# Kernel tuning notes

Hardware: AMD Instinct MI355X
Metric: run time of the kernel (lower is better)

Reference implementation:

```python
import jax, jax.numpy as jnp
import numpy as np

F_NODES = 360        # nodes per graph == num_features (square connectome)
NUM_GRAPHS = 128
NUM_EDGES = 1_000_000
C = 128              # hidden_channels
NUM_LAYERS = 3
HIDDEN = 512
NUM_CLASSES = 2
EPS = 1e-5


def _bn(x, g, b):
    # BatchNorm1d in training mode: biased batch statistics over the batch dim.
    m = x.mean(axis=0)
    v = x.var(axis=0)
    return (x - m) * jax.lax.rsqrt(v + EPS) * g + b


def _gcn(x, W, b, src, dst):
    # GCNConv: x' = D^{-1/2} (A + I) D^{-1/2} (x W) + b
    N = x.shape[0]
    h = x @ W                                   # [N, C]
    loop = jnp.arange(N, dtype=src.dtype)
    src2 = jnp.concatenate([src, loop])
    dst2 = jnp.concatenate([dst, loop])
    deg = jax.ops.segment_sum(jnp.ones_like(dst2, dtype=h.dtype), dst2, num_segments=N)
    dinv = jnp.where(deg > 0, jax.lax.rsqrt(deg), 0.0)
    norm = dinv[src2] * dinv[dst2]              # [E+N]
    out = jax.ops.segment_sum(h[src2] * norm[:, None], dst2, num_segments=N)
    return out + b


def setup_inputs() -> dict:
    key = jax.random.key(0)
    ks = jax.random.split(key, 16)
    N = NUM_GRAPHS * F_NODES
    x = jax.random.normal(ks[0], (N, F_NODES), jnp.float32)
    # edges confined within each graph
    g = jax.random.randint(ks[1], (NUM_EDGES,), 0, NUM_GRAPHS)
    edge_src = g * F_NODES + jax.random.randint(ks[2], (NUM_EDGES,), 0, F_NODES)
    edge_dst = g * F_NODES + jax.random.randint(ks[3], (NUM_EDGES,), 0, F_NODES)
    batch = jnp.repeat(jnp.arange(NUM_GRAPHS), F_NODES)

    def lin(k, fi, fo):
        s = 1.0 / np.sqrt(fi)
        return jax.random.uniform(k, (fi, fo), jnp.float32, -s, s)

    input_dim = F_NODES * (F_NODES + 1) // 2    # 64980
    input_dim1 = input_dim + C * NUM_LAYERS     # 65364
    H2 = HIDDEN // 2
    params = dict(
        Wc1=lin(ks[4], F_NODES, C), bc1=jnp.zeros((C,), jnp.float32),
        Wc2=lin(ks[5], C, C), bc2=jnp.zeros((C,), jnp.float32),
        Wc3=lin(ks[6], C, C), bc3=jnp.zeros((C,), jnp.float32),
        bn_g=jnp.ones((input_dim,), jnp.float32), bn_b=jnp.zeros((input_dim,), jnp.float32),
        bnh_g=jnp.ones((C * NUM_LAYERS,), jnp.float32), bnh_b=jnp.zeros((C * NUM_LAYERS,), jnp.float32),
        W1=lin(ks[7], input_dim1, HIDDEN), b1=jnp.zeros((HIDDEN,), jnp.float32),
        g1=jnp.ones((HIDDEN,), jnp.float32), be1=jnp.zeros((HIDDEN,), jnp.float32),
        W2=lin(ks[8], HIDDEN, H2), b2=jnp.zeros((H2,), jnp.float32),
        g2=jnp.ones((H2,), jnp.float32), be2=jnp.zeros((H2,), jnp.float32),
        W3=lin(ks[9], H2, H2), b3=jnp.zeros((H2,), jnp.float32),
        g3=jnp.ones((H2,), jnp.float32), be3=jnp.zeros((H2,), jnp.float32),
        W4=lin(ks[10], H2, NUM_CLASSES), b4=jnp.zeros((NUM_CLASSES,), jnp.float32),
    )
    return {"x": x, "edge_src": edge_src, "edge_dst": edge_dst, "batch": batch, **params}


def reference(x, edge_src, edge_dst, batch,
              Wc1, bc1, Wc2, bc2, Wc3, bc3,
              bn_g, bn_b, bnh_g, bnh_b,
              W1, b1, g1, be1, W2, b2, g2, be2, W3, b3, g3, be3, W4, b4):
    N, F = x.shape
    B = N // F                                   # nodes per graph == F
    # stacked GCN convs with tanh
    xs = [x]
    for W, b in ((Wc1, bc1), (Wc2, bc2), (Wc3, bc3)):
        xs.append(jnp.tanh(_gcn(xs[-1], W, b, edge_src, edge_dst)))
    # per-graph upper-triangular gather of the raw connectome (vectorized)
    iu0, iu1 = np.triu_indices(F)
    x0 = xs[0].reshape(B, F, F)[:, iu0, iu1]     # [B, F(F+1)/2]
    x0 = _bn(x0, bn_g, bn_b)
    # per-layer segment-mean pooling over graphs
    cnt = jax.ops.segment_sum(jnp.ones((N,), x.dtype), batch, num_segments=B)
    h = jnp.concatenate(
        [jax.ops.segment_sum(xx, batch, num_segments=B) / cnt[:, None] for xx in xs[1:]],
        axis=1)                                  # [B, C*num_layers]
    h = _bn(h, bnh_g, bnh_b)
    z = jnp.concatenate([x0, h], axis=1)         # [B, input_dim1]
    # MLP head (dropout in eval mode => identity)
    z = jax.nn.relu(_bn(z @ W1 + b1, g1, be1))
    z = jax.nn.relu(_bn(z @ W2 + b2, g2, be2))
    z = jax.nn.relu(_bn(z @ W3 + b3, g3, be3))
    return jax.nn.log_softmax(z @ W4 + b4, axis=1)
```

## Files before the change

kernel.cpp:

```cpp
#include <hip/hip_runtime.h>
#include <hip/hip_bf16.h>
#include <math.h>

#define FN 360
#define NG 128
#define NN 46080
#define CH 128
#define NE 1000000
#define TRI 64980
#define D1 65364
#define ZLD 65376
#define H1 512
#define H2 256
#define EPS 1e-5f
#define NSPLIT 64
#define NB1 720
#define ERNG 8192
#define NR 123
#define NCH 8
#define CROWS 45
#define SBCAP 32

typedef unsigned short u16;
typedef __attribute__((ext_vector_type(8))) short bf16x8;
typedef __attribute__((ext_vector_type(4))) float f32x4;

__device__ __forceinline__ float bf2f(u16 v) {
  union { unsigned u; float f; } x; x.u = ((unsigned)v) << 16; return x.f;
}
__device__ __forceinline__ u16 f2bf(float f) {
  union { float f; unsigned u; } x; x.f = f;
  unsigned r = x.u + 0x7fffu + ((x.u >> 16) & 1u);
  return (u16)(r >> 16);
}
__device__ __forceinline__ bf16x8 bzero8() {
  bf16x8 z;
#pragma unroll
  for (int j = 0; j < 8; j++) z[j] = 0;
  return z;
}

static const size_t Z_OFF    = 0;
static const size_t PART_OFF = 16736256;
static const size_t EBUF_OFF = PART_OFF;
static const size_t CNT_OFF  = PART_OFF + 16121856;
static const size_t Y1_OFF   = 50290688;
static const size_t A1_OFF   = 50552832;
static const size_t A2_OFF   = 50683904;
static const size_t A3_OFF   = 50749440;
static const size_t DEG_OFF  = 66355200;
static const size_t HP_OFF   = 66539520;
static const size_t AB_OFF   = 66740224;
static const size_t PT_OFF   = 99917824;
static const size_t H_OFF    = 111714304;

__global__ __launch_bounds__(256) void k_gemm1deg(
    const float* __restrict__ X, const float* __restrict__ W,
    u16* __restrict__ PT,
    const int* __restrict__ src, const int* __restrict__ dst,
    float* __restrict__ deg, unsigned* __restrict__ ebuf, int* __restrict__ cnt) {
  if (blockIdx.x >= NB1) {
    __shared__ int cur[NG * NCH];
    int r = blockIdx.x - NB1;
    for (int i = threadIdx.x; i < NG * NCH; i += 256) cur[i] = 0;
    __syncthreads();
    int base = r * ERNG;
#pragma unroll 4
    for (int it = 0; it < ERNG / 256; it++) {
      int e = base + it * 256 + threadIdx.x;
      if (e < NE) {
        int s = src[e], d = dst[e];
        atomicAdd(&deg[d], 1.0f);
        int g = d / FN;
        int ls = s - g * FN, ld = d - g * FN;
        int gc = g * NCH + ld / CROWS;
        int slot = atomicAdd(&cur[gc], 1);
        if (slot < SBCAP)
          ebuf[((size_t)r * (NG * NCH) + gc) * SBCAP + slot] =
              (unsigned)ls | ((unsigned)ld << 16);
      }
    }
    __syncthreads();
    for (int i = threadIdx.x; i < NG * NCH; i += 256)
      cnt[r * (NG * NCH) + i] = cur[i];
    return;
  }
  __shared__ __attribute__((aligned(16))) u16 WT[128][40];
  const int K = FN;
  int wid = threadIdx.x >> 6, lane = threadIdx.x & 63;
  int quad = lane >> 4, l16 = lane & 15;
  int m0 = blockIdx.x * 64 + (wid & 1) * 32;
  int n0w = (wid >> 1) * 64;
  int kl = threadIdx.x >> 3, nseg = (threadIdx.x & 7) * 16;
  f32x4 acc[2][4];
#pragma unroll
  for (int i = 0; i < 2; i++)
#pragma unroll
    for (int j = 0; j < 4; j++) acc[i][j] = (f32x4){0,0,0,0};
  for (int k0 = 0; k0 < K; k0 += 32) {
    __syncthreads();
    int kg = k0 + kl;
    if (kg < K) {
      const float* wrow = W + (size_t)kg * CH + nseg;
      f32x4 w0 = *(const f32x4*)(wrow);
      f32x4 w1 = *(const f32x4*)(wrow + 4);
      f32x4 w2 = *(const f32x4*)(wrow + 8);
      f32x4 w3 = *(const f32x4*)(wrow + 12);
#pragma unroll
      for (int j = 0; j < 4; j++) {
        WT[nseg + j][kl]      = f2bf(w0[j]);
        WT[nseg + 4 + j][kl]  = f2bf(w1[j]);
        WT[nseg + 8 + j][kl]  = f2bf(w2[j]);
        WT[nseg + 12 + j][kl] = f2bf(w3[j]);
      }
    } else {
#pragma unroll
      for (int j = 0; j < 16; j++) WT[nseg + j][kl] = 0;
    }
    __syncthreads();
    int kk = k0 + quad * 8;
    bool kin = kk < K;
    bf16x8 af[2];
#pragma unroll
    for (int tm = 0; tm < 2; tm++) {
      int row = m0 + tm * 16 + l16;
      bf16x8 a = bzero8();
      if (kin) {
        f32x4 va = *(const f32x4*)(X + (size_t)row * K + kk);
        f32x4 vb = *(const f32x4*)(X + (size_t)row * K + kk + 4);
#pragma unroll
        for (int j = 0; j < 4; j++) { a[j] = (short)f2bf(va[j]); a[4 + j] = (short)f2bf(vb[j]); }
      }
      af[tm] = a;
    }
    bf16x8 bfr[4];
#pragma unroll
    for (int tn = 0; tn < 4; tn++)
      bfr[tn] = *(const bf16x8*)&WT[n0w + tn * 16 + l16][quad * 8];
#pragma unroll
    for (int tm = 0; tm < 2; tm++)
#pragma unroll
      for (int tn = 0; tn < 4; tn++)
        acc[tm][tn] = __builtin_amdgcn_mfma_f32_16x16x32_bf16(af[tm], bfr[tn], acc[tm][tn], 0, 0, 0);
  }
#pragma unroll
  for (int tm = 0; tm < 2; tm++)
#pragma unroll
    for (int tn = 0; tn < 4; tn++) {
      int col = n0w + tn * 16 + l16;
      int rowb = m0 + tm * 16 + quad * 4;
#pragma unroll
      for (int r = 0; r < 4; r++) {
        int row = rowb + r;
        int g = row / FN, lr = row - g * FN;
        PT[((size_t)g * CH + col) * FN + lr] = f2bf(acc[tm][tn][r]);
      }
    }
}

__global__ __launch_bounds__(256) void k_abuild3(
    const unsigned* __restrict__ ebuf, const int* __restrict__ cnt,
    const float* __restrict__ deg, u16* __restrict__ Ab) {
  __shared__ __attribute__((aligned(16))) float sA[CROWS * FN];
  __shared__ int scnt[NR];
  int g = blockIdx.x >> 3, ch = blockIdx.x & 7;
  int gc = g * NCH + ch;
  int r0 = ch * CROWS;
  for (int i = threadIdx.x; i < CROWS * FN / 4; i += 256) ((f32x4*)sA)[i] = (f32x4){0,0,0,0};
  for (int i = threadIdx.x; i < NR; i += 256) scnt[i] = cnt[i * (NG * NCH) + gc];
  __syncthreads();
  const float* dg = deg + g * FN;
  for (int idx = threadIdx.x; idx < NR * SBCAP; idx += 256) {
    int r = idx >> 5, sl = idx & (SBCAP - 1);
    if (sl < scnt[r]) {
      unsigned p = ebuf[((size_t)r * (NG * NCH) + gc) * SBCAP + sl];
      int ls = (int)(p & 0xffffu), ld = (int)(p >> 16);
      float w = rsqrtf(dg[ls] + 1.0f) * rsqrtf(dg[ld] + 1.0f);
      atomicAdd(&sA[(ld - r0) * FN + ls], w);
    }
  }
  __syncthreads();
  if (threadIdx.x < CROWS) {
    int l = r0 + threadIdx.x;
    float dv = rsqrtf(dg[l] + 1.0f);
    sA[threadIdx.x * FN + l] += dv * dv;
  }
  __syncthreads();
  unsigned* dstu = (unsigned*)(Ab + (size_t)g * FN * FN + (size_t)r0 * FN);
  for (int i = threadIdx.x; i < CROWS * FN / 2; i += 256) {
    unsigned lo = f2bf(sA[2 * i]), hi = f2bf(sA[2 * i + 1]);
    dstu[i] = lo | (hi << 16);
  }
}

template<bool GUARD>
__device__ __forceinline__ void gbig_body(
    const u16* __restrict__ Z, const float* __restrict__ W1f,
    float* __restrict__ part, int s, int n0b) {
  __shared__ __attribute__((aligned(16))) u16 WT[128][40];
  int wid = threadIdx.x >> 6, lane = threadIdx.x & 63;
  int quad = lane >> 4, l16 = lane & 15;
  int m0 = wid * 32;
  int kl = threadIdx.x >> 3, nseg = (threadIdx.x & 7) * 16;
  int kbeg = s * 1024;
  int kend = GUARD ? ((ZLD < kbeg + 1024) ? ZLD : (kbeg + 1024)) : (kbeg + 1024);
  f32x4 acc[2][8];
#pragma unroll
  for (int i = 0; i < 2; i++)
#pragma unroll
    for (int j = 0; j < 8; j++) acc[i][j] = (f32x4){0,0,0,0};
  for (int k0 = kbeg; k0 < kend; k0 += 32) {
    __syncthreads();
    int kg = k0 + kl;
    if (!GUARD || kg < D1) {
      const float* wrow = W1f + (size_t)kg * H1 + n0b + nseg;
      f32x4 w0 = *(const f32x4*)(wrow);
      f32x4 w1 = *(const f32x4*)(wrow + 4);
      f32x4 w2 = *(const f32x4*)(wrow + 8);
      f32x4 w3 = *(const f32x4*)(wrow + 12);
#pragma unroll
      for (int j = 0; j < 4; j++) {
        WT[nseg + j][kl]      = f2bf(w0[j]);
        WT[nseg + 4 + j][kl]  = f2bf(w1[j]);
        WT[nseg + 8 + j][kl]  = f2bf(w2[j]);
        WT[nseg + 12 + j][kl] = f2bf(w3[j]);
      }
    } else {
#pragma unroll
      for (int j = 0; j < 16; j++) WT[nseg + j][kl] = 0;
    }
    __syncthreads();
    int kk = k0 + quad * 8;
    bf16x8 af[2];
#pragma unroll
    for (int tm = 0; tm < 2; tm++) {
      int row = m0 + tm * 16 + l16;
      af[tm] = *(const bf16x8*)(Z + (size_t)row * ZLD + kk);
    }
    bf16x8 bfr[8];
#pragma unroll
    for (int tn = 0; tn < 8; tn++)
      bfr[tn] = *(const bf16x8*)&WT[tn * 16 + l16][quad * 8];
#pragma unroll
    for (int tm = 0; tm < 2; tm++)
#pragma unroll
      for (int tn = 0; tn < 8; tn++)
        acc[tm][tn] = __builtin_amdgcn_mfma_f32_16x16x32_bf16(af[tm], bfr[tn], acc[tm][tn], 0, 0, 0);
  }
#pragma unroll
  for (int tm = 0; tm < 2; tm++)
#pragma unroll
    for (int tn = 0; tn < 8; tn++) {
      int col = n0b + tn * 16 + l16;
      int rowb = m0 + tm * 16 + quad * 4;
#pragma unroll
      for (int r = 0; r < 4; r++)
        part[((size_t)s * NG + rowb + r) * H1 + col] = acc[tm][tn][r];
    }
}

__global__ __launch_bounds__(256) void k_agg(
    const u16* __restrict__ Ab, const u16* __restrict__ PT,
    const float* __restrict__ bias, u16* __restrict__ Hout,
    float* __restrict__ hp, int loff,
    const u16* __restrict__ Z, const float* __restrict__ W1f,
    float* __restrict__ part) {
  if (blockIdx.x >= NG * 6) {
    int id2 = blockIdx.x - NG * 6;
    gbig_body<false>(Z, W1f, part, id2 >> 2, (id2 & 3) * 128);
    return;
  }
  __shared__ float ps[8][128];
  int id = blockIdx.x;
  int g = (id & 7) + 8 * (id / 48);
  int mb = (id % 48) >> 3;
  int wid = threadIdx.x >> 6, lane = threadIdx.x & 63;
  int quad = lane >> 4, l16 = lane & 15;
  int m0 = mb * 64 + (wid & 1) * 32;
  int n0 = (wid >> 1) * 64;
  const u16* Abg = Ab + (size_t)g * FN * FN;
  const u16* PTg = PT + (size_t)g * CH * FN;
  f32x4 acc[2][4];
#pragma unroll
  for (int i = 0; i < 2; i++)
#pragma unroll
    for (int j = 0; j < 4; j++) acc[i][j] = (f32x4){0,0,0,0};
  for (int k0 = 0; k0 < FN; k0 += 32) {
    int kk = k0 + quad * 8;
    bool kin = kk < FN;
    bf16x8 af[2];
#pragma unroll
    for (int tm = 0; tm < 2; tm++) {
      int row = m0 + tm * 16 + l16;
      af[tm] = (kin && row < FN) ? *(const bf16x8*)(Abg + (size_t)row * FN + kk) : bzero8();
    }
    bf16x8 bfr[4];
#pragma unroll
    for (int tn = 0; tn < 4; tn++) {
      int col = n0 + tn * 16 + l16;
      bfr[tn] = kin ? *(const bf16x8*)(PTg + (size_t)col * FN + kk) : bzero8();
    }
#pragma unroll
    for (int tm = 0; tm < 2; tm++)
#pragma unroll
      for (int tn = 0; tn < 4; tn++)
        acc[tm][tn] = __builtin_amdgcn_mfma_f32_16x16x32_bf16(af[tm], bfr[tn], acc[tm][tn], 0, 0, 0);
  }
  float lsum[4] = {0.f, 0.f, 0.f, 0.f};
#pragma unroll
  for (int tm = 0; tm < 2; tm++)
#pragma unroll
    for (int tn = 0; tn < 4; tn++) {
      int col = n0 + tn * 16 + l16;
      float bc = bias[col];
      int rowb = m0 + tm * 16 + quad * 4;
#pragma unroll
      for (int r = 0; r < 4; r++) {
        int row = rowb + r;
        if (row < FN) {
          float t = tanhf(acc[tm][tn][r] + bc);
          if (Hout) Hout[(size_t)(g * FN + row) * CH + col] = f2bf(t);
          lsum[tn] += t;
        }
      }
    }
  int cid = (wid & 1) * 4 + quad;
#pragma unroll
  for (int tn = 0; tn < 4; tn++) ps[cid][n0 + tn * 16 + l16] = lsum[tn];
  __syncthreads();
  if (threadIdx.x < 128) {
    float s = 0.f;
#pragma unroll
    for (int c = 0; c < 8; c++) s += ps[c][threadIdx.x];
    atomicAdd(&hp[g * 384 + loff + threadIdx.x], s);
  }
}

__global__ __launch_bounds__(256) void k_gemm_xw_bf16(
    const u16* __restrict__ X, const float* __restrict__ W,
    u16* __restrict__ PT) {
  __shared__ __attribute__((aligned(16))) u16 WT[128][40];
  int wid = threadIdx.x >> 6, lane = threadIdx.x & 63;
  int quad = lane >> 4, l16 = lane & 15;
  int m0 = blockIdx.x * 64 + (wid & 1) * 32;
  int n0w = (wid >> 1) * 64;
  int kl = threadIdx.x >> 3, nseg = (threadIdx.x & 7) * 16;
  f32x4 acc[2][4];
#pragma unroll
  for (int i = 0; i < 2; i++)
#pragma unroll
    for (int j = 0; j < 4; j++) acc[i][j] = (f32x4){0,0,0,0};
  for (int k0 = 0; k0 < CH; k0 += 32) {
    __syncthreads();
    int kg = k0 + kl;
    const float* wrow = W + (size_t)kg * CH + nseg;
    f32x4 w0 = *(const f32x4*)(wrow);
    f32x4 w1 = *(const f32x4*)(wrow + 4);
    f32x4 w2 = *(const f32x4*)(wrow + 8);
    f32x4 w3 = *(const f32x4*)(wrow + 12);
#pragma unroll
    for (int j = 0; j < 4; j++) {
      WT[nseg + j][kl]      = f2bf(w0[j]);
      WT[nseg + 4 + j][kl]  = f2bf(w1[j]);
      WT[nseg + 8 + j][kl]  = f2bf(w2[j]);
      WT[nseg + 12 + j][kl] = f2bf(w3[j]);
    }
    __syncthreads();
    int kk = k0 + quad * 8;
    bf16x8 af[2];
#pragma unroll
    for (int tm = 0; tm < 2; tm++) {
      int row = m0 + tm * 16 + l16;
      af[tm] = *(const bf16x8*)(X + (size_t)row * CH + kk);
    }
    bf16x8 bfr[4];
#pragma unroll
    for (int tn = 0; tn < 4; tn++)
      bfr[tn] = *(const bf16x8*)&WT[n0w + tn * 16 + l16][quad * 8];
#pragma unroll
    for (int tm = 0; tm < 2; tm++)
#pragma unroll
      for (int tn = 0; tn < 4; tn++)
        acc[tm][tn] = __builtin_amdgcn_mfma_f32_16x16x32_bf16(af[tm], bfr[tn], acc[tm][tn], 0, 0, 0);
  }
#pragma unroll
  for (int tm = 0; tm < 2; tm++)
#pragma unroll
    for (int tn = 0; tn < 4; tn++) {
      int col = n0w + tn * 16 + l16;
      int rowb = m0 + tm * 16 + quad * 4;
#pragma unroll
      for (int r = 0; r < 4; r++) {
        int row = rowb + r;
        int g = row / FN, lr = row - g * FN;
        PT[((size_t)g * CH + col) * FN + lr] = f2bf(acc[tm][tn][r]);
      }
    }
}

__global__ __launch_bounds__(256) void k_gemm2tri(
    const u16* __restrict__ X, const float* __restrict__ W,
    u16* __restrict__ PT,
    const float* __restrict__ x, const float* __restrict__ gam,
    const float* __restrict__ bet, u16* __restrict__ z) {
  if (blockIdx.x >= NB1) {
    int i = blockIdx.x - NB1;
    int off = i * FN - (i * (i - 1)) / 2;
    for (int j = i + (int)threadIdx.x; j < FN; j += 256) {
      float s = 0.f, ss = 0.f;
#pragma unroll 8
      for (int b = 0; b < NG; b++) {
        float v = x[(size_t)(b * FN + i) * FN + j];
        s += v; ss += v * v;
      }
      float mean = s * (1.0f / NG);
      float var = fmaxf(ss * (1.0f / NG) - mean * mean, 0.f);
      float rstd = rsqrtf(var + EPS);
      int f = off + (j - i);
      float ga = gam[f] * rstd;
      float bb = bet[f] - mean * ga;
#pragma unroll 8
      for (int b = 0; b < NG; b++) {
        float v = x[(size_t)(b * FN + i) * FN + j];
        z[(size_t)b * ZLD + f] = f2bf(v * ga + bb);
      }
    }
    return;
  }
  __shared__ __attribute__((aligned(16))) u16 WT[128][40];
  int wid = threadIdx.x >> 6, lane = threadIdx.x & 63;
  int quad = lane >> 4, l16 = lane & 15;
  int m0 = blockIdx.x * 64 + (wid & 1) * 32;
  int n0w = (wid >> 1) * 64;
  int kl = threadIdx.x >> 3, nseg = (threadIdx.x & 7) * 16;
  f32x4 acc[2][4];
#pragma unroll
  for (int i = 0; i < 2; i++)
#pragma unroll
    for (int j = 0; j < 4; j++) acc[i][j] = (f32x4){0,0,0,0};
  for (int k0 = 0; k0 < CH; k0 += 32) {
    __syncthreads();
    int kg = k0 + kl;
    const float* wrow = W + (size_t)kg * CH + nseg;
    f32x4 w0 = *(const f32x4*)(wrow);
    f32x4 w1 = *(const f32x4*)(wrow + 4);
    f32x4 w2 = *(const f32x4*)(wrow + 8);
    f32x4 w3 = *(const f32x4*)(wrow + 12);
#pragma unroll
    for (int j = 0; j < 4; j++) {
      WT[nseg + j][kl]      = f2bf(w0[j]);
      WT[nseg + 4 + j][kl]  = f2bf(w1[j]);
      WT[nseg + 8 + j][kl]  = f2bf(w2[j]);
      WT[nseg + 12 + j][kl] = f2bf(w3[j]);
    }
    __syncthreads();
    int kk = k0 + quad * 8;
    bf16x8 af[2];
#pragma unroll
    for (int tm = 0; tm < 2; tm++) {
      int row = m0 + tm * 16 + l16;
      af[tm] = *(const bf16x8*)(X + (size_t)row * CH + kk);
    }
    bf16x8 bfr[4];
#pragma unroll
    for (int tn = 0; tn < 4; tn++)
      bfr[tn] = *(const bf16x8*)&WT[n0w + tn * 16 + l16][quad * 8];
#pragma unroll
    for (int tm = 0; tm < 2; tm++)
#pragma unroll
      for (int tn = 0; tn < 4; tn++)
        acc[tm][tn] = __builtin_amdgcn_mfma_f32_16x16x32_bf16(af[tm], bfr[tn], acc[tm][tn], 0, 0, 0);
  }
#pragma unroll
  for (int tm = 0; tm < 2; tm++)
#pragma unroll
    for (int tn = 0; tn < 4; tn++) {
      int col = n0w + tn * 16 + l16;
      int rowb = m0 + tm * 16 + quad * 4;
#pragma unroll
      for (int r = 0; r < 4; r++) {
        int row = rowb + r;
        int g = row / FN, lr = row - g * FN;
        PT[((size_t)g * CH + col) * FN + lr] = f2bf(acc[tm][tn][r]);
      }
    }
}

__global__ void k_hpbn(const float* __restrict__ hp,
                       const float* __restrict__ hgam, const float* __restrict__ hbet,
                       u16* __restrict__ z) {
  for (int c = threadIdx.x; c < 384; c += 256) {
    float s = 0.f, ss = 0.f;
#pragma unroll 8
    for (int m = 0; m < NG; m++) {
      float v = hp[m * 384 + c] * (1.0f / FN);
      s += v; ss += v * v;
    }
    float mean = s * (1.0f / NG);
    float var = fmaxf(ss * (1.0f / NG) - mean * mean, 0.f);
    float rstd = rsqrtf(var + EPS);
    float ga = hgam[c] * rstd;
    float bb = hbet[c] - mean * ga;
#pragma unroll 8
    for (int m = 0; m < NG; m++)
      z[(size_t)m * ZLD + TRI + c] = f2bf(hp[m * 384 + c] * (1.0f / FN) * ga + bb);
  }
  if (threadIdx.x < NG) {
    for (int t = 0; t < ZLD - D1; t++)
      z[(size_t)threadIdx.x * ZLD + D1 + t] = 0;
  }
}

__global__ __launch_bounds__(256) void k_gbig_tail(
    const u16* __restrict__ Z, const float* __restrict__ W1f, float* __restrict__ part) {
  gbig_body<true>(Z, W1f, part, NSPLIT - 1, blockIdx.x * 128);
}

__global__ void k_red(const float* __restrict__ part, float* __restrict__ y1) {
  int idx = blockIdx.x * 256 + threadIdx.x;
  float s = 0.f;
#pragma unroll 8
  for (int i = 0; i < NSPLIT; i++) s += part[(size_t)i * 65536 + idx];
  y1[idx] = s;
}

__global__ __launch_bounds__(256) void k_bnrelu(
    const float* __restrict__ y, const float* __restrict__ gam,
    const float* __restrict__ bet, u16* __restrict__ a, int N) {
  __shared__ float sb[4][64], sb2[4][64];
  int c63 = threadIdx.x & 63;
  int grp = threadIdx.x >> 6;
  int c = blockIdx.x * 64 + c63;
  float s = 0.f, ss = 0.f;
#pragma unroll 8
  for (int m = grp * 32; m < grp * 32 + 32; m++) {
    float v = y[(size_t)m * N + c]; s += v; ss += v * v;
  }
  sb[grp][c63] = s; sb2[grp][c63] = ss;
  __syncthreads();
  float S = sb[0][c63] + sb[1][c63] + sb[2][c63] + sb[3][c63];
  float SS = sb2[0][c63] + sb2[1][c63] + sb2[2][c63] + sb2[3][c63];
  float mean = S * (1.0f / NG);
  float var = fmaxf(SS * (1.0f / NG) - mean * mean, 0.f);
  float rstd = rsqrtf(var + EPS);
  float ga = gam[c] * rstd;
  float bb = bet[c] - mean * ga;
#pragma unroll 8
  for (int m = grp * 32; m < grp * 32 + 32; m++) {
    float v = y[(size_t)m * N + c] * ga + bb;
    a[(size_t)m * N + c] = f2bf(fmaxf(v, 0.f));
  }
}

__global__ __launch_bounds__(256) void k_mlpbn(
    const u16* __restrict__ A, const float* __restrict__ W,
    const float* __restrict__ gam, const float* __restrict__ bet,
    u16* __restrict__ aout, int K, int N) {
  __shared__ __attribute__((aligned(16))) u16 WT[64][40];
  __shared__ float rs[4][4][4][16], rss[4][4][4][16];
  int wid = threadIdx.x >> 6, lane = threadIdx.x & 63;
  int quad = lane >> 4, l16 = lane & 15;
  int n0b = blockIdx.x * 64;
  int m0 = wid * 32;
  int kl = threadIdx.x >> 3;
  int nseg = (threadIdx.x & 7) * 8;
  f32x4 acc[2][4];
#pragma unroll
  for (int i = 0; i < 2; i++)
#pragma unroll
    for (int j = 0; j < 4; j++) acc[i][j] = (f32x4){0,0,0,0};
  for (int k0 = 0; k0 < K; k0 += 32) {
    __syncthreads();
    const float* wrow = W + (size_t)(k0 + kl) * N + n0b + nseg;
    f32x4 w0 = *(const f32x4*)(wrow);
    f32x4 w1 = *(const f32x4*)(wrow + 4);
#pragma unroll
    for (int j = 0; j < 4; j++) {
      WT[nseg + j][kl]     = f2bf(w0[j]);
      WT[nseg + 4 + j][kl] = f2bf(w1[j]);
    }
    __syncthreads();
    int kk = k0 + quad * 8;
    bf16x8 af[2];
#pragma unroll
    for (int tm = 0; tm < 2; tm++) {
      int row = m0 + tm * 16 + l16;
      af[tm] = *(const bf16x8*)(A + (size_t)row * K + kk);
    }
    bf16x8 bfr[4];
#pragma unroll
    for (int tn = 0; tn < 4; tn++)
      bfr[tn] = *(const bf16x8*)&WT[tn * 16 + l16][quad * 8];
#pragma unroll
    for (int tm = 0; tm < 2; tm++)
#pragma unroll
      for (int tn = 0; tn < 4; tn++)
        acc[tm][tn] = __builtin_amdgcn_mfma_f32_16x16x32_bf16(af[tm], bfr[tn], acc[tm][tn], 0, 0, 0);
  }
  __syncthreads();
#pragma unroll
  for (int tn = 0; tn < 4; tn++) {
    float s = 0.f, ss = 0.f;
#pragma unroll
    for (int tm = 0; tm < 2; tm++)
#pragma unroll
      for (int r = 0; r < 4; r++) { float v = acc[tm][tn][r]; s += v; ss += v * v; }
    rs[wid][quad][tn][l16] = s;
    rss[wid][quad][tn][l16] = ss;
  }
  __syncthreads();
#pragma unroll
  for (int tn = 0; tn < 4; tn++) {
    float S = 0.f, SS = 0.f;
#pragma unroll
    for (int w = 0; w < 4; w++)
#pragma unroll
      for (int q = 0; q < 4; q++) { S += rs[w][q][tn][l16]; SS += rss[w][q][tn][l16]; }
    float mean = S * (1.0f / NG);
    float var = fmaxf(SS * (1.0f / NG) - mean * mean, 0.f);
    float rstd = rsqrtf(var + EPS);
    int col = n0b + tn * 16 + l16;
    float ga = gam[col] * rstd;
    float bb = bet[col] - mean * ga;
#pragma unroll
    for (int tm = 0; tm < 2; tm++) {
      int rowb = m0 + tm * 16 + quad * 4;
#pragma unroll
      for (int r = 0; r < 4; r++) {
        float v = acc[tm][tn][r] * ga + bb;
        aout[(size_t)(rowb + r) * N + col] = f2bf(fmaxf(v, 0.f));
      }
    }
  }
}

__global__ void k_head(const u16* __restrict__ a3, const float* __restrict__ W4,
                       const float* __restrict__ b4, float* __restrict__ out) {
  __shared__ float w4s[H2 * 2];
  int m = threadIdx.x;
  for (int i = m; i < H2 * 2; i += 128) w4s[i] = W4[i];
  __syncthreads();
  float a0 = b4[0], a1 = b4[1];
  for (int k0 = 0; k0 < H2; k0 += 8) {
    bf16x8 v = *(const bf16x8*)(a3 + (size_t)m * H2 + k0);
#pragma unroll
    for (int j = 0; j < 8; j++) {
      float f = bf2f((u16)v[j]);
      a0 += f * w4s[(k0 + j) * 2];
      a1 += f * w4s[(k0 + j) * 2 + 1];
    }
  }
  float mx = fmaxf(a0, a1);
  float lse = mx + logf(expf(a0 - mx) + expf(a1 - mx));
  out[m * 2]     = a0 - lse;
  out[m * 2 + 1] = a1 - lse;
}

extern "C" void kernel_launch(void* const* d_in, const int* in_sizes, int n_in,
                              void* d_out, int out_size, void* d_ws, size_t ws_size,
                              hipStream_t stream) {
  const float* x    = (const float*)d_in[0];
  const int* esrc   = (const int*)d_in[1];
  const int* edst   = (const int*)d_in[2];
  const float* Wc1 = (const float*)d_in[4];  const float* bc1 = (const float*)d_in[5];
  const float* Wc2 = (const float*)d_in[6];  const float* bc2 = (const float*)d_in[7];
  const float* Wc3 = (const float*)d_in[8];  const float* bc3 = (const float*)d_in[9];
  const float* bn_g = (const float*)d_in[10]; const float* bn_b = (const float*)d_in[11];
  const float* bnh_g = (const float*)d_in[12]; const float* bnh_b = (const float*)d_in[13];
  const float* W1 = (const float*)d_in[14];
  const float* g1 = (const float*)d_in[16]; const float* be1 = (const float*)d_in[17];
  const float* W2 = (const float*)d_in[18];
  const float* g2 = (const float*)d_in[20]; const float* be2 = (const float*)d_in[21];
  const float* W3 = (const float*)d_in[22];
  const float* g3 = (const float*)d_in[24]; const float* be3 = (const float*)d_in[25];
  const float* W4 = (const float*)d_in[26]; const float* b4 = (const float*)d_in[27];

  char* ws = (char*)d_ws;
  float* deg  = (float*)(ws + DEG_OFF);
  float* hp   = (float*)(ws + HP_OFF);
  u16*   Ab   = (u16*)(ws + AB_OFF);
  unsigned* ebuf = (unsigned*)(ws + EBUF_OFF);
  int*   cnt  = (int*)(ws + CNT_OFF);
  u16*   PT   = (u16*)(ws + PT_OFF);
  u16*   h    = (u16*)(ws + H_OFF);
  u16*   z    = (u16*)(ws + Z_OFF);
  float* part = (float*)(ws + PART_OFF);
  float* y1   = (float*)(ws + Y1_OFF);
  u16*   a1   = (u16*)(ws + A1_OFF);
  u16*   a2   = (u16*)(ws + A2_OFF);
  u16*   a3   = (u16*)(ws + A3_OFF);

  (void)hipMemsetAsync(deg, 0, (size_t)NN * 4 + (size_t)NG * 384 * 4, stream);

  dim3 b256(256);
  k_gemm1deg<<<dim3(NB1 + NR), b256, 0, stream>>>(x, Wc1, PT, esrc, edst, deg, ebuf, cnt);
  k_abuild3<<<dim3(NG * NCH), b256, 0, stream>>>(ebuf, cnt, deg, Ab);
  k_agg<<<dim3(NG * 6), b256, 0, stream>>>(Ab, PT, bc1, h, hp, 0, z, W1, part);
  k_gemm2tri<<<dim3(NB1 + FN), b256, 0, stream>>>(h, Wc2, PT, x, bn_g, bn_b, z);
  k_agg<<<dim3(NG * 6 + 252), b256, 0, stream>>>(Ab, PT, bc2, h, hp, CH, z, W1, part);
  k_gemm_xw_bf16<<<dim3(NB1), b256, 0, stream>>>(h, Wc3, PT);
  k_agg<<<dim3(NG * 6), b256, 0, stream>>>(Ab, PT, bc3, (u16*)nullptr, hp, 2 * CH, z, W1, part);
  k_hpbn<<<dim3(1), b256, 0, stream>>>(hp, bnh_g, bnh_b, z);
  k_gbig_tail<<<dim3(4), b256, 0, stream>>>(z, W1, part);
  k_red<<<dim3(65536 / 256), b256, 0, stream>>>(part, y1);
  k_bnrelu<<<dim3(H1 / 64), b256, 0, stream>>>(y1, g1, be1, a1, H1);
  k_mlpbn<<<dim3(H2 / 64), b256, 0, stream>>>(a1, W2, g2, be2, a2, H1, H2);
  k_mlpbn<<<dim3(H2 / 64), b256, 0, stream>>>(a2, W3, g3, be3, a3, H2, H2);
  k_head<<<dim3(1), dim3(128), 0, stream>>>(a3, W4, b4, (float*)d_out);
}
```

Baseline: 670.5 us.

## Compact edge bins with overflow list and LDS-tiled aggregation GEMM

Edge binning now stores 16-bit packed local indices in bins of 16 per block-chunk, with a shared overflow list spilled to a global overflow buffer. The adjacency build scans that buffer and caches rsqrt degrees in LDS. This shrinks the edge buffer and removes the redundant per-edge rsqrt. The aggregation GEMM switches to 128x128 tiles staged through LDS with register prefetch of the next k-slice, halving block count and increasing reuse. The risk is that every abuild block scans the whole global overflow list, and any edges beyond the overflow caps are silently dropped.

```diff
diff --git a/kernel.cpp b/kernel.cpp
--- a/kernel.cpp
+++ b/kernel.cpp
@@ -19,7 +19,10 @@
 #define NR 123
 #define NCH 8
 #define CROWS 45
-#define SBCAP 32
+#define BCAP 16
+#define OVCAP 192
+#define OVGCAP 32768
+#define NAGG 384
 
 typedef unsigned short u16;
 typedef __attribute__((ext_vector_type(8))) short bf16x8;
@@ -43,13 +46,15 @@
 static const size_t Z_OFF    = 0;
 static const size_t PART_OFF = 16736256;
 static const size_t EBUF_OFF = PART_OFF;
-static const size_t CNT_OFF  = PART_OFF + 16121856;
+static const size_t CNT_OFF  = PART_OFF + 4027392;
+static const size_t OVF_OFF  = CNT_OFF + 503808;
 static const size_t Y1_OFF   = 50290688;
 static const size_t A1_OFF   = 50552832;
 static const size_t A2_OFF   = 50683904;
 static const size_t A3_OFF   = 50749440;
 static const size_t DEG_OFF  = 66355200;
 static const size_t HP_OFF   = 66539520;
+static const size_t OVN_OFF  = 66736128;
 static const size_t AB_OFF   = 66740224;
 static const size_t PT_OFF   = 99917824;
 static const size_t H_OFF    = 111714304;
@@ -58,11 +63,16 @@
     const float* __restrict__ X, const float* __restrict__ W,
     u16* __restrict__ PT,
     const int* __restrict__ src, const int* __restrict__ dst,
-    float* __restrict__ deg, unsigned* __restrict__ ebuf, int* __restrict__ cnt) {
+    float* __restrict__ deg, u16* __restrict__ ebuf, int* __restrict__ cnt,
+    int* __restrict__ govn, unsigned* __restrict__ govf) {
   if (blockIdx.x >= NB1) {
     __shared__ int cur[NG * NCH];
+    __shared__ u16 bins[NG * NCH][BCAP];
+    __shared__ unsigned ovf[OVCAP];
+    __shared__ int ovn, obase;
     int r = blockIdx.x - NB1;
     for (int i = threadIdx.x; i < NG * NCH; i += 256) cur[i] = 0;
+    if (threadIdx.x == 0) ovn = 0;
     __syncthreads();
     int base = r * ERNG;
 #pragma unroll 4
@@ -73,16 +83,35 @@
         atomicAdd(&deg[d], 1.0f);
         int g = d / FN;
         int ls = s - g * FN, ld = d - g * FN;
-        int gc = g * NCH + ld / CROWS;
+        int ch = ld / CROWS;
+        int gc = g * NCH + ch;
         int slot = atomicAdd(&cur[gc], 1);
-        if (slot < SBCAP)
-          ebuf[((size_t)r * (NG * NCH) + gc) * SBCAP + slot] =
-              (unsigned)ls | ((unsigned)ld << 16);
-      }
-    }
-    __syncthreads();
-    for (int i = threadIdx.x; i < NG * NCH; i += 256)
-      cnt[r * (NG * NCH) + i] = cur[i];
+        if (slot < BCAP) {
+          bins[gc][slot] = (u16)(ls | ((ld - ch * CROWS) << 9));
+        } else {
+          int o = atomicAdd(&ovn, 1);
+          if (o < OVCAP) ovf[o] = (unsigned)ls | ((unsigned)ld << 9) | ((unsigned)g << 18);
+        }
+      }
+    }
+    __syncthreads();
+    {
+      const f32x4* sb = (const f32x4*)bins;
+      f32x4* gb = (f32x4*)(ebuf + (size_t)r * (NG * NCH) * BCAP);
+      for (int i = threadIdx.x; i < NG * NCH * BCAP / 8; i += 256) gb[i] = sb[i];
+    }
+    for (int i = threadIdx.x; i < NG * NCH; i += 256) {
+      int c = cur[i];
+      cnt[r * (NG * NCH) + i] = c < BCAP ? c : BCAP;
+    }
+    if (threadIdx.x == 0) {
+      int n = ovn < OVCAP ? ovn : OVCAP;
+      obase = atomicAdd(govn, n);
+    }
+    __syncthreads();
+    int n = ovn < OVCAP ? ovn : OVCAP;
+    for (int i = threadIdx.x; i < n; i += 256)
+      if (obase + i < OVGCAP) govf[obase + i] = ovf[i];
     return;
   }
   __shared__ __attribute__((aligned(16))) u16 WT[128][40];
@@ -159,30 +188,42 @@
 }
 
 __global__ __launch_bounds__(256) void k_abuild3(
-    const unsigned* __restrict__ ebuf, const int* __restrict__ cnt,
+    const u16* __restrict__ ebuf, const int* __restrict__ cnt,
+    const int* __restrict__ govn, const unsigned* __restrict__ govf,
     const float* __restrict__ deg, u16* __restrict__ Ab) {
   __shared__ __attribute__((aligned(16))) float sA[CROWS * FN];
+  __shared__ float sdg[FN];
   __shared__ int scnt[NR];
   int g = blockIdx.x >> 3, ch = blockIdx.x & 7;
   int gc = g * NCH + ch;
   int r0 = ch * CROWS;
   for (int i = threadIdx.x; i < CROWS * FN / 4; i += 256) ((f32x4*)sA)[i] = (f32x4){0,0,0,0};
+  for (int i = threadIdx.x; i < FN; i += 256) sdg[i] = rsqrtf(deg[g * FN + i] + 1.0f);
   for (int i = threadIdx.x; i < NR; i += 256) scnt[i] = cnt[i * (NG * NCH) + gc];
   __syncthreads();
-  const float* dg = deg + g * FN;
-  for (int idx = threadIdx.x; idx < NR * SBCAP; idx += 256) {
-    int r = idx >> 5, sl = idx & (SBCAP - 1);
+  for (int idx = threadIdx.x; idx < NR * BCAP; idx += 256) {
+    int r = idx >> 4, sl = idx & (BCAP - 1);
     if (sl < scnt[r]) {
-      unsigned p = ebuf[((size_t)r * (NG * NCH) + gc) * SBCAP + sl];
-      int ls = (int)(p & 0xffffu), ld = (int)(p >> 16);
-      float w = rsqrtf(dg[ls] + 1.0f) * rsqrtf(dg[ld] + 1.0f);
-      atomicAdd(&sA[(ld - r0) * FN + ls], w);
+      u16 p = ebuf[((size_t)r * (NG * NCH) + gc) * BCAP + sl];
+      int ls = p & 511, ldr = (p >> 9) & 63;
+      atomicAdd(&sA[ldr * FN + ls], sdg[ls] * sdg[r0 + ldr]);
+    }
+  }
+  int on = *govn; if (on > OVGCAP) on = OVGCAP;
+  for (int i = threadIdx.x; i < on; i += 256) {
+    unsigned p = govf[i];
+    if ((int)(p >> 18) == g) {
+      int ld = (p >> 9) & 511, lr = ld - r0;
+      if ((unsigned)lr < (unsigned)CROWS) {
+        int ls = p & 511;
+        atomicAdd(&sA[lr * FN + ls], sdg[ls] * sdg[ld]);
+      }
     }
   }
   __syncthreads();
   if (threadIdx.x < CROWS) {
     int l = r0 + threadIdx.x;
-    float dv = rsqrtf(dg[l] + 1.0f);
+    float dv = sdg[l];
     sA[threadIdx.x * FN + l] += dv * dv;
   }
   __syncthreads();
@@ -265,68 +306,91 @@
     float* __restrict__ hp, int loff,
     const u16* __restrict__ Z, const float* __restrict__ W1f,
     float* __restrict__ part) {
-  if (blockIdx.x >= NG * 6) {
-    int id2 = blockIdx.x - NG * 6;
+  if (blockIdx.x >= NAGG) {
+    int id2 = blockIdx.x - NAGG;
     gbig_body<false>(Z, W1f, part, id2 >> 2, (id2 & 3) * 128);
     return;
   }
+  __shared__ __attribute__((aligned(16))) u16 sA[128][40];
+  __shared__ __attribute__((aligned(16))) u16 sP[128][40];
   __shared__ float ps[8][128];
   int id = blockIdx.x;
-  int g = (id & 7) + 8 * (id / 48);
-  int mb = (id % 48) >> 3;
+  int g = (id & 7) + 8 * (id / 24);
+  int mb = (id % 24) >> 3;
+  int m0blk = mb * 128;
   int wid = threadIdx.x >> 6, lane = threadIdx.x & 63;
   int quad = lane >> 4, l16 = lane & 15;
-  int m0 = mb * 64 + (wid & 1) * 32;
-  int n0 = (wid >> 1) * 64;
+  int mw = (wid & 1) * 64, nw = (wid >> 1) * 64;
   const u16* Abg = Ab + (size_t)g * FN * FN;
   const u16* PTg = PT + (size_t)g * CH * FN;
-  f32x4 acc[2][4];
-#pragma unroll
-  for (int i = 0; i < 2; i++)
+  int t = threadIdx.x;
+  f32x4 acc[4][4];
+#pragma unroll
+  for (int i = 0; i < 4; i++)
 #pragma unroll
     for (int j = 0; j < 4; j++) acc[i][j] = (f32x4){0,0,0,0};
-  for (int k0 = 0; k0 < FN; k0 += 32) {
-    int kk = k0 + quad * 8;
-    bool kin = kk < FN;
-    bf16x8 af[2];
-#pragma unroll
-    for (int tm = 0; tm < 2; tm++) {
-      int row = m0 + tm * 16 + l16;
-      af[tm] = (kin && row < FN) ? *(const bf16x8*)(Abg + (size_t)row * FN + kk) : bzero8();
-    }
-    bf16x8 bfr[4];
+  bf16x8 ra[2], rp[2];
+#define AGG_LOAD(k0)                                                          \
+  {                                                                           \
+    _Pragma("unroll")                                                         \
+    for (int i = 0; i < 2; i++) {                                             \
+      int lin = i * 256 + t;                                                  \
+      int row = lin >> 2, q = lin & 3;                                        \
+      int kg = (k0) + q * 8;                                                  \
+      int grow = m0blk + row;                                                 \
+      ra[i] = (kg < FN && grow < FN)                                          \
+                  ? *(const bf16x8*)(Abg + (size_t)grow * FN + kg) : bzero8();\
+      rp[i] = (kg < FN)                                                       \
+                  ? *(const bf16x8*)(PTg + (size_t)row * FN + kg) : bzero8(); \
+    }                                                                         \
+  }
+  AGG_LOAD(0)
+  for (int step = 0; step < 12; step++) {
+    __syncthreads();
+#pragma unroll
+    for (int i = 0; i < 2; i++) {
+      int lin = i * 256 + t;
+      int row = lin >> 2, q = lin & 3;
+      *(bf16x8*)&sA[row][q * 8] = ra[i];
+      *(bf16x8*)&sP[row][q * 8] = rp[i];
+    }
+    __syncthreads();
+    if (step < 11) AGG_LOAD((step + 1) * 32)
+    bf16x8 af[4], bp[4];
+#pragma unroll
+    for (int tm = 0; tm < 4; tm++)
+      af[tm] = *(const bf16x8*)&sA[mw + tm * 16 + l16][quad * 8];
+#pragma unroll
+    for (int tn = 0; tn < 4; tn++)
+      bp[tn] = *(const bf16x8*)&sP[nw + tn * 16 + l16][quad * 8];
+#pragma unroll
+    for (int tm = 0; tm < 4; tm++)
+#pragma unroll
+      for (int tn = 0; tn < 4; tn++)
+        acc[tm][tn] = __builtin_amdgcn_mfma_f32_16x16x32_bf16(af[tm], bp[tn], acc[tm][tn], 0, 0, 0);
+  }
+#undef AGG_LOAD
+  float lsum[4] = {0.f, 0.f, 0.f, 0.f};
+#pragma unroll
+  for (int tm = 0; tm < 4; tm++)
 #pragma unroll
     for (int tn = 0; tn < 4; tn++) {
-      int col = n0 + tn * 16 + l16;
-      bfr[tn] = kin ? *(const bf16x8*)(PTg + (size_t)col * FN + kk) : bzero8();
-    }
-#pragma unroll
-    for (int tm = 0; tm < 2; tm++)
-#pragma unroll
-      for (int tn = 0; tn < 4; tn++)
-        acc[tm][tn] = __builtin_amdgcn_mfma_f32_16x16x32_bf16(af[tm], bfr[tn], acc[tm][tn], 0, 0, 0);
-  }
-  float lsum[4] = {0.f, 0.f, 0.f, 0.f};
-#pragma unroll
-  for (int tm = 0; tm < 2; tm++)
-#pragma unroll
-    for (int tn = 0; tn < 4; tn++) {
-      int col = n0 + tn * 16 + l16;
+      int col = nw + tn * 16 + l16;
       float bc = bias[col];
-      int rowb = m0 + tm * 16 + quad * 4;
+      int rowb = m0blk + mw + tm * 16 + quad * 4;
 #pragma unroll
       for (int r = 0; r < 4; r++) {
         int row = rowb + r;
         if (row < FN) {
-          float t = tanhf(acc[tm][tn][r] + bc);
-          if (Hout) Hout[(size_t)(g * FN + row) * CH + col] = f2bf(t);
-          lsum[tn] += t;
+          float tt = tanhf(acc[tm][tn][r] + bc);
+          if (Hout) Hout[(size_t)(g * FN + row) * CH + col] = f2bf(tt);
+          lsum[tn] += tt;
         }
       }
     }
   int cid = (wid & 1) * 4 + quad;
 #pragma unroll
-  for (int tn = 0; tn < 4; tn++) ps[cid][n0 + tn * 16 + l16] = lsum[tn];
+  for (int tn = 0; tn < 4; tn++) ps[cid][nw + tn * 16 + l16] = lsum[tn];
   __syncthreads();
   if (threadIdx.x < 128) {
     float s = 0.f;
@@ -678,9 +742,11 @@
   char* ws = (char*)d_ws;
   float* deg  = (float*)(ws + DEG_OFF);
   float* hp   = (float*)(ws + HP_OFF);
+  int*   govn = (int*)(ws + OVN_OFF);
   u16*   Ab   = (u16*)(ws + AB_OFF);
-  unsigned* ebuf = (unsigned*)(ws + EBUF_OFF);
+  u16*   ebuf = (u16*)(ws + EBUF_OFF);
   int*   cnt  = (int*)(ws + CNT_OFF);
+  unsigned* govf = (unsigned*)(ws + OVF_OFF);
   u16*   PT   = (u16*)(ws + PT_OFF);
   u16*   h    = (u16*)(ws + H_OFF);
   u16*   z    = (u16*)(ws + Z_OFF);
@@ -690,16 +756,16 @@
   u16*   a2   = (u16*)(ws + A2_OFF);
   u16*   a3   = (u16*)(ws + A3_OFF);
 
-  (void)hipMemsetAsync(deg, 0, (size_t)NN * 4 + (size_t)NG * 384 * 4, stream);
+  (void)hipMemsetAsync(deg, 0, (size_t)NN * 4 + (size_t)NG * 384 * 4 + 4, stream);
 
   dim3 b256(256);
-  k_gemm1deg<<<dim3(NB1 + NR), b256, 0, stream>>>(x, Wc1, PT, esrc, edst, deg, ebuf, cnt);
-  k_abuild3<<<dim3(NG * NCH), b256, 0, stream>>>(ebuf, cnt, deg, Ab);
-  k_agg<<<dim3(NG * 6), b256, 0, stream>>>(Ab, PT, bc1, h, hp, 0, z, W1, part);
+  k_gemm1deg<<<dim3(NB1 + NR), b256, 0, stream>>>(x, Wc1, PT, esrc, edst, deg, ebuf, cnt, govn, govf);
+  k_abuild3<<<dim3(NG * NCH), b256, 0, stream>>>(ebuf, cnt, govn, govf, deg, Ab);
+  k_agg<<<dim3(NAGG), b256, 0, stream>>>(Ab, PT, bc1, h, hp, 0, z, W1, part);
   k_gemm2tri<<<dim3(NB1 + FN), b256, 0, stream>>>(h, Wc2, PT, x, bn_g, bn_b, z);
-  k_agg<<<dim3(NG * 6 + 252), b256, 0, stream>>>(Ab, PT, bc2, h, hp, CH, z, W1, part);
+  k_agg<<<dim3(NAGG + 252), b256, 0, stream>>>(Ab, PT, bc2, h, hp, CH, z, W1, part);
   k_gemm_xw_bf16<<<dim3(NB1), b256, 0, stream>>>(h, Wc3, PT);
-  k_agg<<<dim3(NG * 6), b256, 0, stream>>>(Ab, PT, bc3, (u16*)nullptr, hp, 2 * CH, z, W1, part);
+  k_agg<<<dim3(NAGG), b256, 0, stream>>>(Ab, PT, bc3, (u16*)nullptr, hp, 2 * CH, z, W1, part);
   k_hpbn<<<dim3(1), b256, 0, stream>>>(hp, bnh_g, bnh_b, z);
   k_gbig_tail<<<dim3(4), b256, 0, stream>>>(z, W1, part);
   k_red<<<dim3(65536 / 256), b256, 0, stream>>>(part, y1);
```

Result: faster. 617.2 us (-7.9%).
